# Performance work log

Measured on AMD Instinct MI355X. Metric: run time of the kernel, lower is better.

## Reference

```python
import jax, jax.numpy as jnp
import numpy as np

HIDDEN = 1024
INTER = 4096
N_EXPERTS = 8
TOP_K = 2
INIT_STD = 0.02


def setup_inputs() -> dict:
    key = jax.random.key(0)
    ks = jax.random.split(key, 6)
    x = jax.random.normal(ks[0], (2, 1024, HIDDEN), dtype=jnp.float32)
    Wg = jax.random.normal(ks[1], (N_EXPERTS, HIDDEN), dtype=jnp.float32) * INIT_STD
    # Expert MLP params, stacked over experts. W1: [E, H, I], W2: [E, I, H].
    W1 = jax.random.normal(ks[2], (N_EXPERTS, HIDDEN, INTER), dtype=jnp.float32) * INIT_STD
    b1 = jnp.zeros((N_EXPERTS, INTER), dtype=jnp.float32)
    W2 = jax.random.normal(ks[3], (N_EXPERTS, INTER, HIDDEN), dtype=jnp.float32) * INIT_STD
    b2 = jnp.zeros((N_EXPERTS, HIDDEN), dtype=jnp.float32)
    return {"x": x, "Wg": Wg, "W1": W1, "b1": b1, "W2": W2, "b2": b2}


def reference(x, Wg, W1, b1, W2, b2):
    orig_shape = x.shape
    xt = x.reshape(-1, HIDDEN)              # [T, H]
    T = xt.shape[0]

    # Gating: top-k logits -> softmax over the k selected experts.
    logits = xt @ Wg.T                      # [T, E]
    topk_logits, topk_idx = jax.lax.top_k(logits, TOP_K)   # [T, K]
    w = jax.nn.softmax(topk_logits, axis=-1)               # [T, K]

    # Scatter top-k weights into a dense [T, E] gate matrix (zeros elsewhere).
    rows = jnp.arange(T)[:, None]
    gates = jnp.zeros((T, N_EXPERTS), xt.dtype).at[rows, topk_idx].add(w)

    # Dense expert compute (mathematically identical: non-selected experts get
    # gate weight 0). Expert MLP: Linear -> GELU (exact, erf) -> Linear.
    h = jnp.einsum('th,ehi->tei', xt, W1) + b1             # [T, E, I]
    h = jax.nn.gelu(h, approximate=False)
    o = jnp.einsum('tei,eih->teh', h, W2) + b2             # [T, E, H]
    y = jnp.einsum('te,teh->th', gates, o)                 # [T, H]
    return y.reshape(orig_shape)
```

## Files before the change

kernel.cpp:

```cpp
#include <hip/hip_runtime.h>
#include <hip/hip_bf16.h>

#define HID 1024
#define INTER 4096
#define NE 8
#define NTOK 2048
#define MAXROWS 6144

typedef __attribute__((ext_vector_type(8))) short short8v;
typedef __attribute__((ext_vector_type(4))) short short4v;
typedef __attribute__((ext_vector_type(4))) float f32x4;

__device__ __forceinline__ unsigned short f2bf(float f) {
  unsigned int u = __builtin_bit_cast(unsigned int, f);
  u = (u + 0x7FFFu + ((u >> 16) & 1u)) >> 16;
  return (unsigned short)u;
}
__device__ __forceinline__ float bf2f(unsigned short s) {
  unsigned int u = ((unsigned int)s) << 16;
  return __builtin_bit_cast(float, u);
}

typedef const __attribute__((address_space(1))) unsigned int* gas_t;
typedef __attribute__((address_space(3))) unsigned int* las_t;
__device__ __forceinline__ void gld16(const unsigned short* g, unsigned short* l) {
  __builtin_amdgcn_global_load_lds((gas_t)(const void*)g, (las_t)(void*)l, 16, 0, 0);
}

__device__ __forceinline__ void tconv_tile(const float* __restrict__ in,
                                           unsigned short* __restrict__ out,
                                           int R, int C, int bx, int by, int z,
                                           float* __restrict__ t) {
  const int r0 = by * 64, c0 = bx * 64;
  const int tr = threadIdx.x / 16;
  const int tc = (threadIdx.x % 16) * 4;
  const float* ip = in + ((size_t)z * R + r0) * (size_t)C + c0;
#pragma unroll
  for (int p = 0; p < 4; ++p) {
    f32x4 v = *(const f32x4*)&ip[(size_t)(p * 16 + tr) * C + tc];
    t[(p * 16 + tr) * 65 + tc + 0] = v[0];
    t[(p * 16 + tr) * 65 + tc + 1] = v[1];
    t[(p * 16 + tr) * 65 + tc + 2] = v[2];
    t[(p * 16 + tr) * 65 + tc + 3] = v[3];
  }
  __syncthreads();
  unsigned short* op = out + ((size_t)z * C + c0) * (size_t)R + r0;
#pragma unroll
  for (int p = 0; p < 4; ++p) {
    int c = p * 16 + tr;
    unsigned int a0 = (unsigned int)f2bf(t[(tc + 0) * 65 + c]) |
                      ((unsigned int)f2bf(t[(tc + 1) * 65 + c]) << 16);
    unsigned int a1 = (unsigned int)f2bf(t[(tc + 2) * 65 + c]) |
                      ((unsigned int)f2bf(t[(tc + 3) * 65 + c]) << 16);
    uint2 val; val.x = a0; val.y = a1;
    *(uint2*)&op[(size_t)c * R + tc] = val;
  }
}

__device__ __forceinline__ void wave_tconv2(const float* __restrict__ in,
                                            unsigned short* __restrict__ out,
                                            int gidx, float* __restrict__ sc, int lane) {
  const int e = gidx >> 11;
  const int r = gidx & 2047;
  const int i0 = (r >> 5) * 64, h0 = (r & 31) * 32;
  const float* ip = in + ((size_t)e * INTER + i0) * HID + h0;
  f32x4 v[8];
#pragma unroll
  for (int p = 0; p < 8; ++p)
    v[p] = *(const f32x4*)&ip[(size_t)(p * 8 + (lane >> 3)) * HID + (lane & 7) * 4];
#pragma unroll
  for (int p = 0; p < 8; ++p) {
    const int row = p * 8 + (lane >> 3), col = (lane & 7) * 4;
#pragma unroll
    for (int j = 0; j < 4; ++j) sc[row * 37 + col + j] = v[p][j];
  }
  asm volatile("s_waitcnt lgkmcnt(0)" ::: "memory");
  __builtin_amdgcn_sched_barrier(0);
  unsigned short* op = out + ((size_t)e * HID + h0) * INTER + i0;
#pragma unroll
  for (int p = 0; p < 4; ++p) {
    const int c = p * 8 + (lane >> 3);
    const int r8 = (lane & 7) * 8;
    uint4 w;
    unsigned int* wp = (unsigned int*)&w;
#pragma unroll
    for (int j = 0; j < 4; ++j) {
      unsigned int lo = f2bf(sc[(r8 + 2 * j) * 37 + c]);
      unsigned int hi = f2bf(sc[(r8 + 2 * j + 1) * 37 + c]);
      wp[j] = lo | (hi << 16);
    }
    *(uint4*)&op[(size_t)c * INTER + r8] = w;
  }
}

__global__ __launch_bounds__(256) void prep_kernel(const float* __restrict__ x,
                                                   const float* __restrict__ W1,
                                                   const float* __restrict__ wg,
                                                   unsigned short* __restrict__ xb,
                                                   unsigned short* __restrict__ w1t,
                                                   int* __restrict__ tok_e,
                                                   float* __restrict__ tok_w) {
  __shared__ float sh[64 * 65];
  int bid = blockIdx.x;
  if (bid < 2048) {
    size_t i = (size_t)bid * 256 + threadIdx.x;
    f32x4 v = *(const f32x4*)&x[i * 4];
    uint2 r;
    r.x = (unsigned int)f2bf(v[0]) | ((unsigned int)f2bf(v[1]) << 16);
    r.y = (unsigned int)f2bf(v[2]) | ((unsigned int)f2bf(v[3]) << 16);
    *(uint2*)&xb[i * 4] = r;
    return;
  }
  bid -= 2048;
  if (bid < 8192) {
    tconv_tile(W1, w1t, HID, INTER, bid % 64, (bid / 64) % 16, bid / 1024, sh);
    return;
  }
  bid -= 8192;
  {
    const int t = bid;
    float acc[NE];
#pragma unroll
    for (int e = 0; e < NE; ++e) acc[e] = 0.f;
    for (int k = threadIdx.x; k < HID; k += 256) {
      float xv = x[(size_t)t * HID + k];
#pragma unroll
      for (int e = 0; e < NE; ++e) acc[e] += xv * wg[e * HID + k];
    }
#pragma unroll
    for (int e = 0; e < NE; ++e) {
#pragma unroll
      for (int off = 32; off >= 1; off >>= 1) acc[e] += __shfl_xor(acc[e], off, 64);
    }
    float* red = sh;
    const int wave = threadIdx.x >> 6, lane = threadIdx.x & 63;
    if (lane == 0) {
#pragma unroll
      for (int e = 0; e < NE; ++e) red[wave * NE + e] = acc[e];
    }
    __syncthreads();
    if (threadIdx.x == 0) {
      float l[NE];
#pragma unroll
      for (int e = 0; e < NE; ++e)
        l[e] = red[0 * NE + e] + red[1 * NE + e] + red[2 * NE + e] + red[3 * NE + e];
      int i0 = 0;
#pragma unroll
      for (int e = 1; e < NE; ++e) if (l[e] > l[i0]) i0 = e;
      int i1 = -1;
#pragma unroll
      for (int e = 0; e < NE; ++e) {
        if (e == i0) continue;
        if (i1 < 0 || l[e] > l[i1]) i1 = e;
      }
      float e1 = __expf(l[i1] - l[i0]);
      float w0 = 1.f / (1.f + e1);
      tok_e[t * 2 + 0] = i0;
      tok_e[t * 2 + 1] = i1;
      tok_w[t * 2 + 0] = w0;
      tok_w[t * 2 + 1] = 1.f - w0;
    }
  }
}

__global__ __launch_bounds__(512) void routing_kernel(const int* __restrict__ tok_e,
                                                      int* __restrict__ list_tok,
                                                      int* __restrict__ tok_gslot,
                                                      int* __restrict__ offs_out) {
  __shared__ int cnts[NE];
  __shared__ int offs_s[NE + 1];
  const int e = threadIdx.x >> 6, lane = threadIdx.x & 63;
  int c = 0;
  for (int base = 0; base < NTOK; base += 64) {
    int tok = base + lane;
    int e0 = tok_e[tok * 2], e1 = tok_e[tok * 2 + 1];
    bool m = (e0 == e) || (e1 == e);
    unsigned long long mask = __ballot(m);
    c += __popcll(mask);
  }
  if (lane == 0) cnts[e] = c;
  __syncthreads();
  if (threadIdx.x == 0) {
    int o = 0;
    for (int i = 0; i < NE; ++i) { offs_s[i] = o; o += (cnts[i] + 255) & ~255; }
    offs_s[NE] = o;
    for (int i = 0; i <= NE; ++i) offs_out[i] = offs_s[i];
  }
  __syncthreads();
  const int off = offs_s[e];
  int run = 0;
  for (int base = 0; base < NTOK; base += 64) {
    int tok = base + lane;
    int e0 = tok_e[tok * 2], e1 = tok_e[tok * 2 + 1];
    bool m = (e0 == e) || (e1 == e);
    unsigned long long mask = __ballot(m);
    int pos = run + __popcll(mask & ((1ull << lane) - 1ull));
    if (m) {
      int gs = off + pos;
      list_tok[gs] = tok;
      tok_gslot[tok * 2 + ((e0 == e) ? 0 : 1)] = gs;
    }
    run += __popcll(mask);
  }
  const int cnt = cnts[e];
  const int padded = (cnt + 255) & ~255;
  for (int p = cnt + lane; p < padded; p += 64) list_tok[off + p] = 0;
}

template <int KTOT, int NTOT, bool FIRST, int NSPLIT, bool TCONV>
__global__ __launch_bounds__(512, 2) void moe_gemm(const unsigned short* __restrict__ Abase,
                                                   const unsigned short* __restrict__ Bbase,
                                                   const float* __restrict__ bias,
                                                   const int* __restrict__ list_tok,
                                                   const int* __restrict__ offs,
                                                   void* __restrict__ outp,
                                                   const float* __restrict__ W2f,
                                                   unsigned short* __restrict__ w2t) {
  constexpr int KS = KTOT / NSPLIT;
  constexpr int T = KS / 64;
  constexpr int nM = MAXROWS / 256;
  constexpr int nN = NTOT / 256;
  constexpr int NWG = nM * nN * NSPLIT;
  __shared__ __align__(16) unsigned short lds[65536];

  const int tid = threadIdx.x;
  const int wid = tid >> 6, lane = tid & 63;

  if (TCONV && (int)blockIdx.x >= NWG) {
    wave_tconv2(W2f, w2t, ((int)blockIdx.x - NWG) * 8 + wid,
                (float*)lds + wid * (64 * 37), lane);
    return;
  }

  int wg = blockIdx.x;
  wg = (wg & 7) * (NWG >> 3) + (wg >> 3);
  const int ksid = (NSPLIT > 1) ? (wg / (nM * nN)) : 0;
  const int rem = wg % (nM * nN);
  const int mt = rem % nM;
  const int nt = rem / nM;
  const int grow0 = mt * 256;
  if (grow0 >= offs[NE]) return;
  int e = 0;
#pragma unroll
  for (int i = 1; i < NE; ++i) if (grow0 >= offs[i]) e = i;
  const int n0 = nt * 256;
  const int k0 = ksid * KS;

  const int jsrc = (((tid & 3) ^ ((tid >> 3) & 3)) * 8);
  const unsigned short* ag[2];
  const unsigned short* bg[2];
#pragma unroll
  for (int c = 0; c < 2; ++c) {
    const int R = c * 128 + (tid >> 2);
    size_t arow;
    if (FIRST) arow = (size_t)list_tok[grow0 + R] * KTOT;
    else       arow = (size_t)(grow0 + R) * KTOT;
    ag[c] = Abase + arow + k0 + jsrc;
    bg[c] = Bbase + (size_t)e * NTOT * KTOT + (size_t)(n0 + R) * KTOT + k0 + jsrc;
  }

  const int fr = lane & 15, q4 = lane >> 4;
  const int csw = (q4 ^ ((fr >> 1) & 3)) * 8;
  const int wm = wid >> 2, wn = wid & 3;
  int aoff[4], boff[4];
#pragma unroll
  for (int m = 0; m < 4; ++m) aoff[m] = (wm * 128 + m * 16 + fr) * 32 + csw;
#pragma unroll
  for (int n = 0; n < 4; ++n) boff[n] = 16384 + (wn * 64 + n * 16 + fr) * 32 + csw;

  f32x4 acc[8][4] = {};

#define STG(MAT, KH, D1, TOFF)                                                          \
  {                                                                                     \
    const unsigned short* s0 = ((MAT) ? bg[0] : ag[0]) + (TOFF) + (KH) * 32;            \
    const unsigned short* s1 = ((MAT) ? bg[1] : ag[1]) + (TOFF) + (KH) * 32;            \
    unsigned short* db = lds + (D1) * 32768 + (MAT) * 16384 + (KH) * 8192 + wid * 512;  \
    gld16(s0, db);                                                                      \
    gld16(s1, db + 4096);                                                               \
  }

#define PH(DD, KSS, MH, DOSTG, SMAT, SKH, TOFF)                                         \
  {                                                                                     \
    const unsigned short* Lp = lds + (DD) * 32768 + (KSS) * 8192;                       \
    short8v af[4], bf[4];                                                               \
    _Pragma("unroll")                                                                   \
    for (int m = 0; m < 4; ++m) af[m] = *(const short8v*)&Lp[(MH) * 2048 + aoff[m]];    \
    _Pragma("unroll")                                                                   \
    for (int n = 0; n < 4; ++n) bf[n] = *(const short8v*)&Lp[boff[n]];                  \
    if (DOSTG) STG(SMAT, SKH, (DD) ^ 1, TOFF);                                          \
    asm volatile("s_waitcnt lgkmcnt(0)" ::: "memory");                                  \
    __builtin_amdgcn_sched_barrier(0);                                                  \
    __builtin_amdgcn_s_setprio(1);                                                      \
    _Pragma("unroll")                                                                   \
    for (int n = 0; n < 4; ++n)                                                         \
      _Pragma("unroll")                                                                 \
      for (int m = 0; m < 4; ++m)                                                       \
        acc[(MH) * 4 + m][n] = __builtin_amdgcn_mfma_f32_16x16x32_bf16(                 \
            af[m], bf[n], acc[(MH) * 4 + m][n], 0, 0, 0);                               \
    __builtin_amdgcn_s_setprio(0);                                                      \
  }

  STG(0, 0, 0, 0); STG(1, 0, 0, 0); STG(0, 1, 0, 0); STG(1, 1, 0, 0);
  asm volatile("s_waitcnt vmcnt(4)" ::: "memory");
  asm volatile("s_barrier" ::: "memory");

  for (int t = 0; t < T; ++t) {
    const int d = t & 1;
    const int toff = (t + 1) * 64;
    const bool hn = (t + 1 < T);
    PH(d, 0, 0, hn, 0, 0, toff);
    PH(d, 0, 1, hn, 1, 0, toff);
    if (hn) asm volatile("s_waitcnt vmcnt(4)" ::: "memory");
    else    asm volatile("s_waitcnt vmcnt(0)" ::: "memory");
    asm volatile("s_barrier" ::: "memory");
    PH(d, 1, 0, hn, 0, 1, toff);
    PH(d, 1, 1, hn, 1, 1, toff);
    if (hn) {
      asm volatile("s_waitcnt vmcnt(4)" ::: "memory");
      asm volatile("s_barrier" ::: "memory");
    }
  }

#undef PH
#undef STG

#pragma unroll
  for (int m = 0; m < 8; ++m) {
#pragma unroll
    for (int n = 0; n < 4; ++n) {
      const int gcol = n0 + wn * 64 + n * 16 + fr;
      float bv = 0.f;
      if (FIRST) bv = bias[e * NTOT + gcol];
#pragma unroll
      for (int r = 0; r < 4; ++r) {
        const int grow = grow0 + wm * 128 + m * 16 + q4 * 4 + r;
        float v = acc[m][n][r] + bv;
        if (FIRST) {
          v = 0.5f * v * (1.0f + erff(v * 0.70710678118654752f));
          ((unsigned short*)outp)[(size_t)grow * NTOT + gcol] = f2bf(v);
        } else {
          ((unsigned short*)outp)[((size_t)ksid * MAXROWS + grow) * NTOT + gcol] = f2bf(v);
        }
      }
    }
  }
}

template <int NSPLIT>
__global__ __launch_bounds__(256) void combine_kernel(const unsigned short* __restrict__ part,
                                                      const int* __restrict__ tok_gslot,
                                                      const int* __restrict__ tok_e,
                                                      const float* __restrict__ tok_w,
                                                      const float* __restrict__ b2,
                                                      float* __restrict__ y) {
  const int t = blockIdx.x;
  const int c = threadIdx.x * 4;
  const int gs0 = tok_gslot[t * 2 + 0], gs1 = tok_gslot[t * 2 + 1];
  const int e0 = tok_e[t * 2 + 0], e1 = tok_e[t * 2 + 1];
  const float w0 = tok_w[t * 2 + 0], w1 = tok_w[t * 2 + 1];
  float s0[4] = {0.f, 0.f, 0.f, 0.f}, s1[4] = {0.f, 0.f, 0.f, 0.f};
#pragma unroll
  for (int ks = 0; ks < NSPLIT; ++ks) {
    short4v p0 = *(const short4v*)&part[((size_t)ks * MAXROWS + gs0) * HID + c];
    short4v p1 = *(const short4v*)&part[((size_t)ks * MAXROWS + gs1) * HID + c];
#pragma unroll
    for (int i = 0; i < 4; ++i) {
      s0[i] += bf2f((unsigned short)p0[i]);
      s1[i] += bf2f((unsigned short)p1[i]);
    }
  }
  f32x4 bb0 = *(const f32x4*)&b2[e0 * HID + c];
  f32x4 bb1 = *(const f32x4*)&b2[e1 * HID + c];
  f32x4 r;
#pragma unroll
  for (int i = 0; i < 4; ++i)
    r[i] = w0 * (s0[i] + bb0[i]) + w1 * (s1[i] + bb1[i]);
  *(f32x4*)&y[(size_t)t * HID + c] = r;
}

extern "C" void kernel_launch(void* const* d_in, const int* in_sizes, int n_in,
                              void* d_out, int out_size, void* d_ws, size_t ws_size,
                              hipStream_t stream) {
  const float* x  = (const float*)d_in[0];
  const float* wg = (const float*)d_in[1];
  const float* W1 = (const float*)d_in[2];
  const float* b1 = (const float*)d_in[3];
  const float* W2 = (const float*)d_in[4];
  const float* b2 = (const float*)d_in[5];
  float* y = (float*)d_out;

  unsigned char* ws = (unsigned char*)d_ws;
  size_t off = 0;
  unsigned short* w1t  = (unsigned short*)(ws + off);
  unsigned short* part = (unsigned short*)(ws + off);
  off += (size_t)8 * MAXROWS * HID * 2;
  unsigned short* w2t  = (unsigned short*)(ws + off); off += (size_t)NE * HID * INTER * 2;
  unsigned short* xb   = (unsigned short*)(ws + off); off += (size_t)NTOK * HID * 2;
  unsigned short* h    = (unsigned short*)(ws + off); off += (size_t)MAXROWS * INTER * 2;
  int* tok_e           = (int*)(ws + off);            off += NTOK * 2 * 4;
  float* tok_w         = (float*)(ws + off);          off += NTOK * 2 * 4;
  int* tok_gslot       = (int*)(ws + off);            off += NTOK * 2 * 4;
  int* list_tok        = (int*)(ws + off);            off += MAXROWS * 4;
  int* offs            = (int*)(ws + off);            off += 64;
  (void)ws_size; (void)in_sizes; (void)n_in; (void)out_size;

  prep_kernel<<<2048 + 8192 + 2048, 256, 0, stream>>>(x, W1, wg, xb, w1t, tok_e, tok_w);
  routing_kernel<<<1, 512, 0, stream>>>(tok_e, list_tok, tok_gslot, offs);
  moe_gemm<HID, INTER, true, 1, true>
      <<<(MAXROWS / 256) * (INTER / 256) + 2048, 512, 0, stream>>>(
          xb, w1t, b1, list_tok, offs, (void*)h, W2, w2t);
  moe_gemm<INTER, HID, false, 8, false>
      <<<(MAXROWS / 256) * (HID / 256) * 8, 512, 0, stream>>>(
          h, w2t, b2, list_tok, offs, (void*)part, nullptr, nullptr);
  combine_kernel<8><<<NTOK, 256, 0, stream>>>(part, tok_gslot, tok_e, tok_w, b2, y);
}
```

Measured before the change: 237.3 us.

## Restructure GEMM main loop to whole-tile prefetch with 64-wide swizzled LDS rows

Replaces the fine-grained four-phase K-loop, which interleaved half-tile global-to-LDS loads with MFMA phases and used vmcnt(4) partial waits, with a simpler double-buffered scheme. The full next 64-K tile is issued at the start of each iteration, then two K-chunks of MFMAs run over all 8x4 accumulators, followed by a full vmcnt(0) wait and a barrier. The LDS layout also changes from 32-element half rows to 64-element rows with an 8-way XOR swizzle to avoid bank conflicts. The aim is fewer barriers and waits per tile and larger MFMA batches. In exchange, load latency overlap is coarser, the full waits can stall, and more A fragments are held live in registers.

```diff
diff --git a/kernel.cpp b/kernel.cpp
--- a/kernel.cpp
+++ b/kernel.cpp
@@ -246,83 +246,83 @@
   const int n0 = nt * 256;
   const int k0 = ksid * KS;
 
-  const int jsrc = (((tid & 3) ^ ((tid >> 3) & 3)) * 8);
-  const unsigned short* ag[2];
-  const unsigned short* bg[2];
-#pragma unroll
-  for (int c = 0; c < 2; ++c) {
-    const int R = c * 128 + (tid >> 2);
+  const int srow8 = tid >> 3;
+  const int jsw = ((tid & 7) ^ (srow8 & 7)) * 8;
+  const unsigned short* ag[4];
+  const unsigned short* bg[4];
+#pragma unroll
+  for (int c = 0; c < 4; ++c) {
+    const int R = c * 64 + srow8;
     size_t arow;
     if (FIRST) arow = (size_t)list_tok[grow0 + R] * KTOT;
     else       arow = (size_t)(grow0 + R) * KTOT;
-    ag[c] = Abase + arow + k0 + jsrc;
-    bg[c] = Bbase + (size_t)e * NTOT * KTOT + (size_t)(n0 + R) * KTOT + k0 + jsrc;
+    ag[c] = Abase + arow + k0 + jsw;
+    bg[c] = Bbase + (size_t)e * NTOT * KTOT + (size_t)(n0 + R) * KTOT + k0 + jsw;
   }
 
   const int fr = lane & 15, q4 = lane >> 4;
-  const int csw = (q4 ^ ((fr >> 1) & 3)) * 8;
   const int wm = wid >> 2, wn = wid & 3;
-  int aoff[4], boff[4];
-#pragma unroll
-  for (int m = 0; m < 4; ++m) aoff[m] = (wm * 128 + m * 16 + fr) * 32 + csw;
-#pragma unroll
-  for (int n = 0; n < 4; ++n) boff[n] = 16384 + (wn * 64 + n * 16 + fr) * 32 + csw;
+  int aoff[8], boff[4];
+#pragma unroll
+  for (int m = 0; m < 8; ++m) {
+    const int row = wm * 128 + m * 16 + fr;
+    aoff[m] = row * 64 + ((q4 ^ (row & 7)) * 8);
+  }
+#pragma unroll
+  for (int n = 0; n < 4; ++n) {
+    const int row = wn * 64 + n * 16 + fr;
+    boff[n] = row * 64 + ((q4 ^ (row & 7)) * 8);
+  }
 
   f32x4 acc[8][4] = {};
 
-#define STG(MAT, KH, D1, TOFF)                                                          \
-  {                                                                                     \
-    const unsigned short* s0 = ((MAT) ? bg[0] : ag[0]) + (TOFF) + (KH) * 32;            \
-    const unsigned short* s1 = ((MAT) ? bg[1] : ag[1]) + (TOFF) + (KH) * 32;            \
-    unsigned short* db = lds + (D1) * 32768 + (MAT) * 16384 + (KH) * 8192 + wid * 512;  \
-    gld16(s0, db);                                                                      \
-    gld16(s1, db + 4096);                                                               \
-  }
-
-#define PH(DD, KSS, MH, DOSTG, SMAT, SKH, TOFF)                                         \
-  {                                                                                     \
-    const unsigned short* Lp = lds + (DD) * 32768 + (KSS) * 8192;                       \
-    short8v af[4], bf[4];                                                               \
-    _Pragma("unroll")                                                                   \
-    for (int m = 0; m < 4; ++m) af[m] = *(const short8v*)&Lp[(MH) * 2048 + aoff[m]];    \
-    _Pragma("unroll")                                                                   \
-    for (int n = 0; n < 4; ++n) bf[n] = *(const short8v*)&Lp[boff[n]];                  \
-    if (DOSTG) STG(SMAT, SKH, (DD) ^ 1, TOFF);                                          \
-    asm volatile("s_waitcnt lgkmcnt(0)" ::: "memory");                                  \
-    __builtin_amdgcn_sched_barrier(0);                                                  \
-    __builtin_amdgcn_s_setprio(1);                                                      \
-    _Pragma("unroll")                                                                   \
-    for (int n = 0; n < 4; ++n)                                                         \
-      _Pragma("unroll")                                                                 \
-      for (int m = 0; m < 4; ++m)                                                       \
-        acc[(MH) * 4 + m][n] = __builtin_amdgcn_mfma_f32_16x16x32_bf16(                 \
-            af[m], bf[n], acc[(MH) * 4 + m][n], 0, 0, 0);                               \
-    __builtin_amdgcn_s_setprio(0);                                                      \
-  }
-
-  STG(0, 0, 0, 0); STG(1, 0, 0, 0); STG(0, 1, 0, 0); STG(1, 1, 0, 0);
-  asm volatile("s_waitcnt vmcnt(4)" ::: "memory");
+#define STAGE(TT, D)                                                         \
+  {                                                                          \
+    _Pragma("unroll")                                                        \
+    for (int c = 0; c < 4; ++c) {                                            \
+      gld16(ag[c] + (TT) * 64, lds + (D) * 32768 + (c * 64 + wid * 8) * 64); \
+      gld16(bg[c] + (TT) * 64,                                               \
+            lds + (D) * 32768 + 16384 + (c * 64 + wid * 8) * 64);            \
+    }                                                                        \
+  }
+
+#define KKC(D, KK)                                                             \
+  {                                                                            \
+    const unsigned short* La = lds + (D) * 32768;                              \
+    const unsigned short* Lb = La + 16384;                                     \
+    short8v af[8], bf[4];                                                      \
+    _Pragma("unroll")                                                          \
+    for (int m = 0; m < 8; ++m) af[m] = *(const short8v*)&La[aoff[m] ^ ((KK) * 32)]; \
+    _Pragma("unroll")                                                          \
+    for (int n = 0; n < 4; ++n) bf[n] = *(const short8v*)&Lb[boff[n] ^ ((KK) * 32)]; \
+    asm volatile("s_waitcnt lgkmcnt(0)" ::: "memory");                         \
+    __builtin_amdgcn_sched_barrier(0);                                         \
+    __builtin_amdgcn_s_setprio(1);                                             \
+    _Pragma("unroll")                                                          \
+    for (int n = 0; n < 4; ++n)                                                \
+      _Pragma("unroll")                                                        \
+      for (int m = 0; m < 8; ++m)                                              \
+        acc[m][n] = __builtin_amdgcn_mfma_f32_16x16x32_bf16(af[m], bf[n], acc[m][n], 0, 0, 0); \
+    __builtin_amdgcn_s_setprio(0);                                             \
+  }
+
+  STAGE(0, 0);
+  asm volatile("s_waitcnt vmcnt(0)" ::: "memory");
   asm volatile("s_barrier" ::: "memory");
 
   for (int t = 0; t < T; ++t) {
     const int d = t & 1;
-    const int toff = (t + 1) * 64;
-    const bool hn = (t + 1 < T);
-    PH(d, 0, 0, hn, 0, 0, toff);
-    PH(d, 0, 1, hn, 1, 0, toff);
-    if (hn) asm volatile("s_waitcnt vmcnt(4)" ::: "memory");
-    else    asm volatile("s_waitcnt vmcnt(0)" ::: "memory");
-    asm volatile("s_barrier" ::: "memory");
-    PH(d, 1, 0, hn, 0, 1, toff);
-    PH(d, 1, 1, hn, 1, 1, toff);
-    if (hn) {
-      asm volatile("s_waitcnt vmcnt(4)" ::: "memory");
+    if (t + 1 < T) STAGE(t + 1, d ^ 1);
+    KKC(d, 0);
+    KKC(d, 1);
+    if (t + 1 < T) {
+      asm volatile("s_waitcnt vmcnt(0)" ::: "memory");
       asm volatile("s_barrier" ::: "memory");
     }
   }
 
-#undef PH
-#undef STG
+#undef KKC
+#undef STAGE
 
 #pragma unroll
   for (int m = 0; m < 8; ++m) {
```

Measured after the change: 225.3 us. 5.0% less time.
